# Performance work log

Measured on AMD Instinct MI355X. Metric: run time of the kernel, lower is better.

The kernel has to match this reference:

```python
import jax, jax.numpy as jnp
import numpy as np

D = 128
N = 131072


def setup_inputs() -> dict:
    key = jax.random.key(0)
    k1, k2 = jax.random.split(key)
    x = jax.random.normal(k1, (N, D), dtype=jnp.float32)
    n_pairs = D * (D - 1) // 2  # 8128
    theta = jax.random.normal(k2, (n_pairs,), dtype=jnp.float32) * 0.1
    # itertools.combinations(range(D), 2) order == row-major upper-triangle order
    ii, jj = np.triu_indices(D, k=1)
    pairs = jnp.stack([jnp.asarray(ii, jnp.int32), jnp.asarray(jj, jnp.int32)], axis=1)
    return {"x": x, "theta": theta, "pairs": pairs}


def reference(x, theta, pairs):
    # x @ G_transpose(D,i,j,th) only changes columns i and j:
    #   col_i' = c*col_i - s*col_j ; col_j' = s*col_i + c*col_j
    # Apply the 2x2 rotation directly instead of building DxD matrices.
    def step(x, inp):
        ij, th = inp
        i, j = ij[0], ij[1]
        c, s = jnp.cos(th), jnp.sin(th)
        xi = x[:, i]  # [N]
        xj = x[:, j]  # [N]
        x = x.at[:, i].set(c * xi - s * xj)
        x = x.at[:, j].set(s * xi + c * xj)
        return x, None

    out, _ = jax.lax.scan(step, x, (pairs, theta))
    return out
```

## Files before the change

kernel.cpp:

```cpp
#include <hip/hip_runtime.h>
#include <hip/hip_bf16.h>

#define DDIM    128
#define NPAIRS  8128
#define NROWS   131072
#define NCHUNK  64
#define CPAIRS  (NPAIRS / NCHUNK)
#define MATELEM (DDIM * DDIM)

typedef __attribute__((ext_vector_type(8))) short bf16x8;
typedef __attribute__((ext_vector_type(4))) float f32x4;

__device__ inline unsigned short f32_to_bf16_rne(float f) {
    unsigned u = __float_as_uint(f);
    u += 0x7fffu + ((u >> 16) & 1u);
    return (unsigned short)(u >> 16);
}

__global__ __launch_bounds__(128) void chunk_kernel(
        const float* __restrict__ theta,
        const int*   __restrict__ pairs,
        unsigned short* __restrict__ chunks) {
    __shared__ float  R[DDIM * (DDIM + 1)];
    __shared__ float2 cs[CPAIRS];
    __shared__ int2   ij[CPAIRS];

    const int t  = threadIdx.x;
    const int c  = blockIdx.x;
    const int p0 = c * CPAIRS;

    if (t < CPAIRS) {
        float th = theta[p0 + t];
        cs[t] = make_float2(cosf(th), sinf(th));
        ij[t] = make_int2(pairs[2 * (p0 + t)], pairs[2 * (p0 + t) + 1]);
    }
    float* row = &R[t * (DDIM + 1)];
    for (int q = 0; q < DDIM; ++q) row[q] = (q == t) ? 1.0f : 0.0f;
    __syncthreads();

    int   cur_i = ij[0].x;
    float ri    = row[cur_i];
    for (int p = 0; p < CPAIRS; ++p) {
        int2   v = ij[p];
        float2 a = cs[p];
        if (v.x != cur_i) {
            row[cur_i] = ri;
            cur_i = v.x;
            ri = row[cur_i];
        }
        float rj = row[v.y];
        row[v.y] = fmaf(a.y, ri, a.x * rj);
        ri       = fmaf(a.x, ri, -(a.y * rj));
    }
    row[cur_i] = ri;
    __syncthreads();

    unsigned short* dst = chunks + (size_t)c * MATELEM;
    for (int oi = t; oi < MATELEM; oi += 128)
        dst[oi] = f32_to_bf16_rne(R[(oi >> 7) * (DDIM + 1) + (oi & 127)]);
}

__global__ __launch_bounds__(256) void combine_kernel(
        const unsigned short* __restrict__ src,
        unsigned short* __restrict__ dst, int emit_frag) {
    const int lane = threadIdx.x & 63;
    const int wave = threadIdx.x >> 6;
    const int lrow = lane & 15;
    const int lkhi = lane >> 4;

    const unsigned short* A = src + (size_t)(2 * blockIdx.x) * MATELEM;
    const unsigned short* B = A + MATELEM;

    f32x4 acc[2][8];
    #pragma unroll
    for (int m = 0; m < 2; ++m)
        #pragma unroll
        for (int n = 0; n < 8; ++n)
            acc[m][n] = (f32x4){0.0f, 0.0f, 0.0f, 0.0f};

    #pragma unroll
    for (int kstep = 0; kstep < 4; ++kstep) {
        const int k0 = kstep * 32 + lkhi * 8;
        bf16x8 afr[2];
        #pragma unroll
        for (int m = 0; m < 2; ++m)
            afr[m] = *reinterpret_cast<const bf16x8*>(
                A + (size_t)(wave * 32 + m * 16 + lrow) * DDIM + k0);
        #pragma unroll
        for (int n = 0; n < 8; ++n) {
            union { bf16x8 v; unsigned short u[8]; } ub;
            #pragma unroll
            for (int e = 0; e < 8; ++e)
                ub.u[e] = B[(size_t)(k0 + e) * DDIM + n * 16 + lrow];
            acc[0][n] = __builtin_amdgcn_mfma_f32_16x16x32_bf16(afr[0], ub.v, acc[0][n], 0, 0, 0);
            acc[1][n] = __builtin_amdgcn_mfma_f32_16x16x32_bf16(afr[1], ub.v, acc[1][n], 0, 0, 0);
        }
    }

    if (!emit_frag) {
        unsigned short* out = dst + (size_t)blockIdx.x * MATELEM;
        #pragma unroll
        for (int m = 0; m < 2; ++m)
            #pragma unroll
            for (int r = 0; r < 4; ++r) {
                const int orow = wave * 32 + m * 16 + lkhi * 4 + r;
                #pragma unroll
                for (int n = 0; n < 8; ++n)
                    out[orow * DDIM + n * 16 + lrow] = f32_to_bf16_rne(acc[m][n][r]);
            }
    } else {
        #pragma unroll
        for (int m = 0; m < 2; ++m)
            #pragma unroll
            for (int r = 0; r < 4; ++r) {
                const int k = wave * 32 + m * 16 + lkhi * 4 + r;
                #pragma unroll
                for (int n = 0; n < 8; ++n) {
                    const int col  = n * 16 + lrow;
                    const size_t flat =
                        ((size_t)((col >> 4) * 4 + (k >> 5)) * 64 +
                         ((k >> 3) & 3) * 16 + (col & 15)) * 8 + (k & 7);
                    dst[flat] = f32_to_bf16_rne(acc[m][n][r]);
                }
            }
    }
}

__global__ __launch_bounds__(256) void gemm_kernel(
        const float* __restrict__ x,
        const unsigned short* __restrict__ bfrag,
        float* __restrict__ out) {
    const int lane = threadIdx.x & 63;
    const int wave = threadIdx.x >> 6;
    const int lrow = lane & 15;
    const int lkhi = lane >> 4;
    const long brow = (long)blockIdx.x * 128 + wave * 32;

    f32x4 acc[2][8];
    #pragma unroll
    for (int m = 0; m < 2; ++m)
        #pragma unroll
        for (int n = 0; n < 8; ++n)
            acc[m][n] = (f32x4){0.0f, 0.0f, 0.0f, 0.0f};

    #pragma unroll
    for (int kstep = 0; kstep < 4; ++kstep) {
        const int k0 = kstep * 32 + lkhi * 8;
        bf16x8 afr[2];
        #pragma unroll
        for (int m = 0; m < 2; ++m) {
            const float* src = x + (brow + m * 16 + lrow) * (long)DDIM + k0;
            f32x4 lo = *reinterpret_cast<const f32x4*>(src);
            f32x4 hi = *reinterpret_cast<const f32x4*>(src + 4);
            union { bf16x8 v; unsigned short u[8]; } ua;
            #pragma unroll
            for (int e = 0; e < 4; ++e) {
                ua.u[e]     = f32_to_bf16_rne(lo[e]);
                ua.u[e + 4] = f32_to_bf16_rne(hi[e]);
            }
            afr[m] = ua.v;
        }
        #pragma unroll
        for (int n = 0; n < 8; ++n) {
            bf16x8 bfr = *reinterpret_cast<const bf16x8*>(
                bfrag + ((size_t)(n * 4 + kstep) * 64 + lane) * 8);
            acc[0][n] = __builtin_amdgcn_mfma_f32_16x16x32_bf16(afr[0], bfr, acc[0][n], 0, 0, 0);
            acc[1][n] = __builtin_amdgcn_mfma_f32_16x16x32_bf16(afr[1], bfr, acc[1][n], 0, 0, 0);
        }
    }

    #pragma unroll
    for (int m = 0; m < 2; ++m) {
        #pragma unroll
        for (int r = 0; r < 4; ++r) {
            const long orow = brow + m * 16 + lkhi * 4 + r;
            #pragma unroll
            for (int n = 0; n < 8; ++n) {
                out[orow * DDIM + n * 16 + lrow] = acc[m][n][r];
            }
        }
    }
}

extern "C" void kernel_launch(void* const* d_in, const int* in_sizes, int n_in,
                              void* d_out, int out_size, void* d_ws, size_t ws_size,
                              hipStream_t stream) {
    (void)in_sizes; (void)n_in; (void)out_size; (void)ws_size;
    const float* x     = (const float*)d_in[0];
    const float* theta = (const float*)d_in[1];
    const int*   pairs = (const int*)d_in[2];
    float* out = (float*)d_out;

    unsigned short* bufA = (unsigned short*)d_ws;
    unsigned short* bufB = bufA + (size_t)NCHUNK * MATELEM;
    unsigned short* frag = bufA + (size_t)(NCHUNK + NCHUNK / 2) * MATELEM;

    chunk_kernel<<<NCHUNK, 128, 0, stream>>>(theta, pairs, bufA);
    combine_kernel<<<32, 256, 0, stream>>>(bufA, bufB, 0);
    combine_kernel<<<16, 256, 0, stream>>>(bufB, bufA, 0);
    combine_kernel<<< 8, 256, 0, stream>>>(bufA, bufB, 0);
    combine_kernel<<< 4, 256, 0, stream>>>(bufB, bufA, 0);
    combine_kernel<<< 2, 256, 0, stream>>>(bufA, bufB, 0);
    combine_kernel<<< 1, 256, 0, stream>>>(bufB, frag, 1);
    gemm_kernel<<<NROWS / 128, 256, 0, stream>>>(x, frag, out);
}
```

Baseline: 91.83 us.

## Use split-bf16 hi/lo matrices in tree combine and final GEMM

Stores each chunk rotation matrix as bf16 hi and lo parts, in both row-major and column-major copies, in one in-place buffer. The combine tree and the final GEMM issue extra MFMAs on the lo parts to approximate fp32 precision for the matrix product. Combine now runs 512 threads with vectorised column-major B loads in place of scalar gathers. The GEMM uses nontemporal loads and stores for x and out. The extra MFMAs roughly double the matrix-core work in the GEMM and triple it in the combine tree, trading speed for accuracy.

```diff
diff --git a/kernel.cpp b/kernel.cpp
--- a/kernel.cpp
+++ b/kernel.cpp
@@ -5,22 +5,31 @@
 #define NPAIRS  8128
 #define NROWS   131072
 #define NCHUNK  64
-#define CPAIRS  (NPAIRS / NCHUNK)
-#define MATELEM (DDIM * DDIM)
+#define CPAIRS  127
+#define MATELEM 16384
+#define MSTRIDE (4 * MATELEM)
 
 typedef __attribute__((ext_vector_type(8))) short bf16x8;
 typedef __attribute__((ext_vector_type(4))) float f32x4;
+typedef __attribute__((ext_vector_type(4))) unsigned short u16x4;
 
 __device__ inline unsigned short f32_to_bf16_rne(float f) {
     unsigned u = __float_as_uint(f);
     u += 0x7fffu + ((u >> 16) & 1u);
     return (unsigned short)(u >> 16);
 }
-
-__global__ __launch_bounds__(128) void chunk_kernel(
+__device__ inline float bf16_to_f32(unsigned short h) {
+    return __uint_as_float((unsigned)h << 16);
+}
+__device__ inline void bsplit(float v, unsigned short& hi, unsigned short& lo) {
+    hi = f32_to_bf16_rne(v);
+    lo = f32_to_bf16_rne(v - bf16_to_f32(hi));
+}
+
+__global__ __launch_bounds__(256) void chunk_kernel(
         const float* __restrict__ theta,
         const int*   __restrict__ pairs,
-        unsigned short* __restrict__ chunks) {
+        unsigned short* __restrict__ buf) {
     __shared__ float  R[DDIM * (DDIM + 1)];
     __shared__ float2 cs[CPAIRS];
     __shared__ int2   ij[CPAIRS];
@@ -34,101 +43,105 @@
         cs[t] = make_float2(cosf(th), sinf(th));
         ij[t] = make_int2(pairs[2 * (p0 + t)], pairs[2 * (p0 + t) + 1]);
     }
-    float* row = &R[t * (DDIM + 1)];
-    for (int q = 0; q < DDIM; ++q) row[q] = (q == t) ? 1.0f : 0.0f;
+    if (t < DDIM) {
+        float* row = &R[t * (DDIM + 1)];
+        for (int q = 0; q < DDIM; ++q) row[q] = (q == t) ? 1.0f : 0.0f;
+    }
     __syncthreads();
 
-    int   cur_i = ij[0].x;
-    float ri    = row[cur_i];
-    for (int p = 0; p < CPAIRS; ++p) {
-        int2   v = ij[p];
-        float2 a = cs[p];
-        if (v.x != cur_i) {
-            row[cur_i] = ri;
-            cur_i = v.x;
-            ri = row[cur_i];
-        }
-        float rj = row[v.y];
-        row[v.y] = fmaf(a.y, ri, a.x * rj);
-        ri       = fmaf(a.x, ri, -(a.y * rj));
-    }
-    row[cur_i] = ri;
+    if (t < DDIM) {
+        float* row = &R[t * (DDIM + 1)];
+        int   cur_i = ij[0].x;
+        float ri    = row[cur_i];
+        for (int p = 0; p < CPAIRS; ++p) {
+            int2   v = ij[p];
+            float2 a = cs[p];
+            if (v.x != cur_i) {
+                row[cur_i] = ri;
+                cur_i = v.x;
+                ri = row[cur_i];
+            }
+            float rj = row[v.y];
+            row[v.y] = fmaf(a.y, ri, a.x * rj);
+            ri       = fmaf(a.x, ri, -(a.y * rj));
+        }
+        row[cur_i] = ri;
+    }
     __syncthreads();
 
-    unsigned short* dst = chunks + (size_t)c * MATELEM;
-    for (int oi = t; oi < MATELEM; oi += 128)
-        dst[oi] = f32_to_bf16_rne(R[(oi >> 7) * (DDIM + 1) + (oi & 127)]);
-}
-
-__global__ __launch_bounds__(256) void combine_kernel(
-        const unsigned short* __restrict__ src,
-        unsigned short* __restrict__ dst, int emit_frag) {
+    unsigned short* dst = buf + (size_t)c * MSTRIDE;
+    for (int oi = t; oi < MATELEM; oi += 256) {
+        int r = oi >> 7, q = oi & 127;
+        unsigned short hi, lo;
+        bsplit(R[r * (DDIM + 1) + q], hi, lo);
+        dst[oi]           = hi;
+        dst[MATELEM + oi] = lo;
+    }
+    for (int oi = t; oi < MATELEM; oi += 256) {
+        int q = oi >> 7, r = oi & 127;
+        unsigned short hi, lo;
+        bsplit(R[r * (DDIM + 1) + q], hi, lo);
+        dst[2 * MATELEM + oi] = hi;
+        dst[3 * MATELEM + oi] = lo;
+    }
+}
+
+__global__ __launch_bounds__(512) void combine_kernel(
+        unsigned short* __restrict__ buf, int level) {
     const int lane = threadIdx.x & 63;
     const int wave = threadIdx.x >> 6;
     const int lrow = lane & 15;
     const int lkhi = lane >> 4;
-
-    const unsigned short* A = src + (size_t)(2 * blockIdx.x) * MATELEM;
-    const unsigned short* B = A + MATELEM;
-
-    f32x4 acc[2][8];
-    #pragma unroll
-    for (int m = 0; m < 2; ++m)
-        #pragma unroll
-        for (int n = 0; n < 8; ++n)
-            acc[m][n] = (f32x4){0.0f, 0.0f, 0.0f, 0.0f};
+    const size_t i0 = (size_t)(2 * blockIdx.x) << level;
+    const size_t i1 = i0 + ((size_t)1 << level);
+
+    unsigned short* D = buf + i0 * MSTRIDE;
+    const unsigned short* Bcm = buf + i1 * MSTRIDE + 2 * MATELEM;
+
+    const int row0 = wave * 16;
+    f32x4 acc[8];
+    #pragma unroll
+    for (int n = 0; n < 8; ++n) acc[n] = (f32x4){0.0f, 0.0f, 0.0f, 0.0f};
 
     #pragma unroll
     for (int kstep = 0; kstep < 4; ++kstep) {
         const int k0 = kstep * 32 + lkhi * 8;
-        bf16x8 afr[2];
-        #pragma unroll
-        for (int m = 0; m < 2; ++m)
-            afr[m] = *reinterpret_cast<const bf16x8*>(
-                A + (size_t)(wave * 32 + m * 16 + lrow) * DDIM + k0);
+        const unsigned short* ap = D + (size_t)(row0 + lrow) * DDIM + k0;
+        bf16x8 ahi = *reinterpret_cast<const bf16x8*>(ap);
+        bf16x8 alo = *reinterpret_cast<const bf16x8*>(ap + MATELEM);
         #pragma unroll
         for (int n = 0; n < 8; ++n) {
-            union { bf16x8 v; unsigned short u[8]; } ub;
-            #pragma unroll
-            for (int e = 0; e < 8; ++e)
-                ub.u[e] = B[(size_t)(k0 + e) * DDIM + n * 16 + lrow];
-            acc[0][n] = __builtin_amdgcn_mfma_f32_16x16x32_bf16(afr[0], ub.v, acc[0][n], 0, 0, 0);
-            acc[1][n] = __builtin_amdgcn_mfma_f32_16x16x32_bf16(afr[1], ub.v, acc[1][n], 0, 0, 0);
-        }
-    }
-
-    if (!emit_frag) {
-        unsigned short* out = dst + (size_t)blockIdx.x * MATELEM;
-        #pragma unroll
-        for (int m = 0; m < 2; ++m)
-            #pragma unroll
-            for (int r = 0; r < 4; ++r) {
-                const int orow = wave * 32 + m * 16 + lkhi * 4 + r;
-                #pragma unroll
-                for (int n = 0; n < 8; ++n)
-                    out[orow * DDIM + n * 16 + lrow] = f32_to_bf16_rne(acc[m][n][r]);
-            }
-    } else {
-        #pragma unroll
-        for (int m = 0; m < 2; ++m)
-            #pragma unroll
-            for (int r = 0; r < 4; ++r) {
-                const int k = wave * 32 + m * 16 + lkhi * 4 + r;
-                #pragma unroll
-                for (int n = 0; n < 8; ++n) {
-                    const int col  = n * 16 + lrow;
-                    const size_t flat =
-                        ((size_t)((col >> 4) * 4 + (k >> 5)) * 64 +
-                         ((k >> 3) & 3) * 16 + (col & 15)) * 8 + (k & 7);
-                    dst[flat] = f32_to_bf16_rne(acc[m][n][r]);
-                }
-            }
+            const unsigned short* bp = Bcm + (size_t)(n * 16 + lrow) * DDIM + k0;
+            bf16x8 bhi = *reinterpret_cast<const bf16x8*>(bp);
+            bf16x8 blo = *reinterpret_cast<const bf16x8*>(bp + MATELEM);
+            acc[n] = __builtin_amdgcn_mfma_f32_16x16x32_bf16(ahi, bhi, acc[n], 0, 0, 0);
+            acc[n] = __builtin_amdgcn_mfma_f32_16x16x32_bf16(alo, bhi, acc[n], 0, 0, 0);
+            acc[n] = __builtin_amdgcn_mfma_f32_16x16x32_bf16(ahi, blo, acc[n], 0, 0, 0);
+        }
+    }
+
+    #pragma unroll
+    for (int n = 0; n < 8; ++n) {
+        const int col = n * 16 + lrow;
+        u16x4 chi, clo;
+        #pragma unroll
+        for (int r = 0; r < 4; ++r) {
+            const int orow = row0 + lkhi * 4 + r;
+            unsigned short hi, lo;
+            bsplit(acc[n][r], hi, lo);
+            D[orow * DDIM + col]           = hi;
+            D[MATELEM + orow * DDIM + col] = lo;
+            chi[r] = hi; clo[r] = lo;
+        }
+        const size_t cmoff = 2 * MATELEM + (size_t)col * DDIM + row0 + lkhi * 4;
+        *reinterpret_cast<u16x4*>(D + cmoff)           = chi;
+        *reinterpret_cast<u16x4*>(D + cmoff + MATELEM) = clo;
     }
 }
 
 __global__ __launch_bounds__(256) void gemm_kernel(
         const float* __restrict__ x,
-        const unsigned short* __restrict__ bfrag,
+        const unsigned short* __restrict__ Bcm,
         float* __restrict__ out) {
     const int lane = threadIdx.x & 63;
     const int wave = threadIdx.x >> 6;
@@ -150,8 +163,8 @@
         #pragma unroll
         for (int m = 0; m < 2; ++m) {
             const float* src = x + (brow + m * 16 + lrow) * (long)DDIM + k0;
-            f32x4 lo = *reinterpret_cast<const f32x4*>(src);
-            f32x4 hi = *reinterpret_cast<const f32x4*>(src + 4);
+            f32x4 lo = __builtin_nontemporal_load(reinterpret_cast<const f32x4*>(src));
+            f32x4 hi = __builtin_nontemporal_load(reinterpret_cast<const f32x4*>(src + 4));
             union { bf16x8 v; unsigned short u[8]; } ua;
             #pragma unroll
             for (int e = 0; e < 4; ++e) {
@@ -162,10 +175,13 @@
         }
         #pragma unroll
         for (int n = 0; n < 8; ++n) {
-            bf16x8 bfr = *reinterpret_cast<const bf16x8*>(
-                bfrag + ((size_t)(n * 4 + kstep) * 64 + lane) * 8);
-            acc[0][n] = __builtin_amdgcn_mfma_f32_16x16x32_bf16(afr[0], bfr, acc[0][n], 0, 0, 0);
-            acc[1][n] = __builtin_amdgcn_mfma_f32_16x16x32_bf16(afr[1], bfr, acc[1][n], 0, 0, 0);
+            const unsigned short* bp = Bcm + (size_t)(n * 16 + lrow) * DDIM + k0;
+            bf16x8 bhi = *reinterpret_cast<const bf16x8*>(bp);
+            bf16x8 blo = *reinterpret_cast<const bf16x8*>(bp + MATELEM);
+            acc[0][n] = __builtin_amdgcn_mfma_f32_16x16x32_bf16(afr[0], bhi, acc[0][n], 0, 0, 0);
+            acc[0][n] = __builtin_amdgcn_mfma_f32_16x16x32_bf16(afr[0], blo, acc[0][n], 0, 0, 0);
+            acc[1][n] = __builtin_amdgcn_mfma_f32_16x16x32_bf16(afr[1], bhi, acc[1][n], 0, 0, 0);
+            acc[1][n] = __builtin_amdgcn_mfma_f32_16x16x32_bf16(afr[1], blo, acc[1][n], 0, 0, 0);
         }
     }
 
@@ -176,7 +192,8 @@
             const long orow = brow + m * 16 + lkhi * 4 + r;
             #pragma unroll
             for (int n = 0; n < 8; ++n) {
-                out[orow * DDIM + n * 16 + lrow] = acc[m][n][r];
+                __builtin_nontemporal_store(acc[m][n][r],
+                                            &out[orow * DDIM + n * 16 + lrow]);
             }
         }
     }
@@ -191,16 +208,10 @@
     const int*   pairs = (const int*)d_in[2];
     float* out = (float*)d_out;
 
-    unsigned short* bufA = (unsigned short*)d_ws;
-    unsigned short* bufB = bufA + (size_t)NCHUNK * MATELEM;
-    unsigned short* frag = bufA + (size_t)(NCHUNK + NCHUNK / 2) * MATELEM;
-
-    chunk_kernel<<<NCHUNK, 128, 0, stream>>>(theta, pairs, bufA);
-    combine_kernel<<<32, 256, 0, stream>>>(bufA, bufB, 0);
-    combine_kernel<<<16, 256, 0, stream>>>(bufB, bufA, 0);
-    combine_kernel<<< 8, 256, 0, stream>>>(bufA, bufB, 0);
-    combine_kernel<<< 4, 256, 0, stream>>>(bufB, bufA, 0);
-    combine_kernel<<< 2, 256, 0, stream>>>(bufA, bufB, 0);
-    combine_kernel<<< 1, 256, 0, stream>>>(bufB, frag, 1);
-    gemm_kernel<<<NROWS / 128, 256, 0, stream>>>(x, frag, out);
-}
+    unsigned short* buf = (unsigned short*)d_ws;
+
+    chunk_kernel<<<NCHUNK, 256, 0, stream>>>(theta, pairs, buf);
+    for (int l = 0; l < 6; ++l)
+        combine_kernel<<<(NCHUNK / 2) >> l, 512, 0, stream>>>(buf, l);
+    gemm_kernel<<<NROWS / 128, 256, 0, stream>>>(x, buf + 2 * MATELEM, out);
+}
```

Result: slower. 208.9 us (+127.5%).
